# Optimization experiments

Measured on AMD Instinct MI355X. Metric: run time of the kernel, lower is better.

The kernel has to match this reference:

```python
import jax, jax.numpy as jnp
import numpy as np

NUM_ROUTING_ITERATIONS = 3


def _squash(t, axis=-1):
    # scale * t / ||t||, scale = ||t||^2 / (1 + ||t||^2)
    squared_norm = jnp.sum(t * t, axis=axis, keepdims=True)
    return squared_norm / (1.0 + squared_norm) * t / jnp.sqrt(squared_norm)


def setup_inputs() -> dict:
    key = jax.random.key(0)
    k_x, k_w = jax.random.split(key)
    B, R, C, O, I = 64, 2048, 16, 32, 16
    x = jax.random.normal(k_x, (B, R, I), dtype=jnp.float32)
    W = jax.random.normal(k_w, (R, C, O, I), dtype=jnp.float32)
    return {"x": x, "W": W}


def reference(x, W):
    # u_hat[b,r,c,o] = sum_i W[r,c,o,i] * x[b,r,i]
    u_hat = jnp.einsum('rcoi,bri->brco', W, x)  # [B,R,C,O]
    B, R, C, O = u_hat.shape
    b = jnp.zeros((B, R, C), dtype=u_hat.dtype)  # routing logits
    v = None
    for _ in range(NUM_ROUTING_ITERATIONS):
        c = jax.nn.softmax(b, axis=2)                      # softmax over capsules (dim=2)
        s = jnp.einsum('brc,brco->bro', c, u_hat)          # (c * u_hat).sum(dim=2)
        v = _squash(s, axis=-1)                            # [B,R,O]
        b = b + jnp.einsum('brco,bro->brc', u_hat, v)      # agreement update
    return v
```

## Files before the change

### kernel.cpp

```cpp
#include <hip/hip_runtime.h>

#define R_DIM 2048
#define O_DIM 32
#define I_DIM 16
#define B_DIM 64
#define BB 32

typedef _Float16 half8  __attribute__((ext_vector_type(8)));
typedef float    f32x4  __attribute__((ext_vector_type(4)));

struct SplitH { half8 h1, h2; };

__device__ __forceinline__ SplitH splitf16x8(const float* __restrict__ p) {
    float f[8];
    *(float4*)(f)     = *(const float4*)(p);
    *(float4*)(f + 4) = *(const float4*)(p + 4);
    SplitH r;
    #pragma unroll
    for (int j = 0; j < 4; ++j) {
        const auto a = __builtin_amdgcn_cvt_pkrtz(f[2*j], f[2*j+1]);
        const float r0 = f[2*j]     - (float)a[0];
        const float r1 = f[2*j + 1] - (float)a[1];
        const auto c = __builtin_amdgcn_cvt_pkrtz(r0, r1);
        r.h1[2*j] = (_Float16)a[0]; r.h1[2*j+1] = (_Float16)a[1];
        r.h2[2*j] = (_Float16)c[0]; r.h2[2*j+1] = (_Float16)c[1];
    }
    return r;
}

template<int CTRL>
__device__ __forceinline__ float dpp_mv(float v) {
    int t = __builtin_amdgcn_update_dpp(0, __float_as_int(v), CTRL, 0xf, 0xf, true);
    return __int_as_float(t);
}
__device__ __forceinline__ float row16_sum(float v) {
    v += dpp_mv<0xB1>(v);
    v += dpp_mv<0x4E>(v);
    v += dpp_mv<0x124>(v);
    v += dpp_mv<0x128>(v);
    return v;
}

__device__ __forceinline__ int swaddr(int b, int col) {
    return b * 512 + (col ^ (((b ^ (b >> 2)) & 3) << 3));
}

__global__ __launch_bounds__(512, 4)
void capsule_routing_kernel(const float* __restrict__ x,
                            const float* __restrict__ W,
                            float* __restrict__ out) {
    __shared__ float u_lds[BB * 512];

    const int tid = threadIdx.x;
    const int bid = blockIdx.x;
    const int r   = bid >> 1;
    const int b0  = (bid & 1) * BB;

    {
        const int lane = tid & 63;
        const int w    = tid >> 6;
        const int q    = lane >> 4;
        const int np   = lane & 15;

        const half8 z8 = {0,0,0,0,0,0,0,0};
        SplitH as[2];
        #pragma unroll
        for (int mt = 0; mt < 2; ++mt) {
            as[mt].h1 = z8; as[mt].h2 = z8;
            if (q < 2)
                as[mt] = splitf16x8(x + ((size_t)(b0 + mt * 16 + np) * R_DIM + r) * I_DIM + q * 8);
        }

        const f32x4 zero4 = {0.f, 0.f, 0.f, 0.f};
        #pragma unroll
        for (int t = 0; t < 4; ++t) {
            const int ntile = w * 4 + t;
            SplitH bs; bs.h1 = z8; bs.h2 = z8;
            if (q < 2)
                bs = splitf16x8(W + ((size_t)r * 512 + ntile * 16 + np) * I_DIM + q * 8);

            #pragma unroll
            for (int mt = 0; mt < 2; ++mt) {
                f32x4 a = __builtin_amdgcn_mfma_f32_16x16x32_f16(as[mt].h2, bs.h1, zero4, 0, 0, 0);
                a = __builtin_amdgcn_mfma_f32_16x16x32_f16(as[mt].h1, bs.h2, a, 0, 0, 0);
                a = __builtin_amdgcn_mfma_f32_16x16x32_f16(as[mt].h1, bs.h1, a, 0, 0, 0);
                const int col = ntile * 16 + np;
                #pragma unroll
                for (int reg = 0; reg < 4; ++reg)
                    u_lds[swaddr(mt * 16 + q * 4 + reg, col)] = a[reg];
            }
        }
    }
    __syncthreads();

    {
        const int b = tid >> 4;
        const int j = tid & 15;

        float u2[32];
        #pragma unroll
        for (int c = 0; c < 16; ++c) {
            const float2 v2 = *(const float2*)&u_lds[swaddr(b, c * 32 + 2 * j)];
            u2[2 * c]     = v2.x;
            u2[2 * c + 1] = v2.y;
        }

        float bv[16];
        #pragma unroll
        for (int c = 0; c < 16; ++c) bv[c] = 0.0f;

        float s0 = 0.f, s1 = 0.f, g = 0.f;

        #pragma unroll
        for (int it = 0; it < 3; ++it) {
            if (it == 0) {
                s0 = 0.f; s1 = 0.f;
                #pragma unroll
                for (int c = 0; c < 16; ++c) { s0 += u2[2*c]; s1 += u2[2*c+1]; }
                s0 *= 0.0625f; s1 *= 0.0625f;
            } else {
                float m = bv[0];
                #pragma unroll
                for (int c = 1; c < 16; ++c) m = fmaxf(m, bv[c]);
                float Z = 0.f; s0 = 0.f; s1 = 0.f;
                #pragma unroll
                for (int c = 0; c < 16; ++c) {
                    const float e = __expf(bv[c] - m);
                    Z += e;
                    s0 = fmaf(e, u2[2*c],   s0);
                    s1 = fmaf(e, u2[2*c+1], s1);
                }
                const float rZ = __builtin_amdgcn_rcpf(Z);
                s0 *= rZ; s1 *= rZ;
            }

            const float nn = row16_sum(s0 * s0 + s1 * s1);
            g = sqrtf(nn) * __builtin_amdgcn_rcpf(1.0f + nn);

            if (it < 2) {
                #pragma unroll
                for (int c = 0; c < 16; ++c) {
                    const float t = row16_sum(fmaf(u2[2*c], s0, u2[2*c+1] * s1));
                    bv[c] = fmaf(g, t, bv[c]);
                }
            }
        }

        *(float2*)(out + ((size_t)(b0 + b) * R_DIM + r) * O_DIM + 2 * j)
            = make_float2(g * s0, g * s1);
    }
}

extern "C" void kernel_launch(void* const* d_in, const int* in_sizes, int n_in,
                              void* d_out, int out_size, void* d_ws, size_t ws_size,
                              hipStream_t stream) {
    const float* x   = (const float*)d_in[0];
    const float* W   = (const float*)d_in[1];
    float*       out = (float*)d_out;

    dim3 grid(R_DIM * (B_DIM / BB));
    dim3 block(512);
    hipLaunchKernelGGL(capsule_routing_kernel, grid, block, 0, stream, x, W, out);
}
```

Baseline: 147.8 us.

## Distribute routing logits across lanes with DPP rotate-reduce and halve batch tile

Each of the 16 lanes in a row now owns one capsule's routing logit. The capsule index is skewed by lane so that the agreement reduction becomes a rotating DPP accumulate chain, replacing 16 separate row16_sum butterflies. The weighted sum is handled the same way by rotating the softmax weights. Softmax max and sum use row-wide DPP reductions instead of per-thread loops over 16 logits. The batch tile drops from 32 to 16 with 256-thread blocks, which doubles the grid and reloads W twice as often. The intent is to cut cross-lane reduction instructions and register pressure.

```diff
diff --git a/kernel.cpp b/kernel.cpp
--- a/kernel.cpp
+++ b/kernel.cpp
@@ -4,7 +4,7 @@
 #define O_DIM 32
 #define I_DIM 16
 #define B_DIM 64
-#define BB 32
+#define BB 16
 
 typedef _Float16 half8  __attribute__((ext_vector_type(8)));
 typedef float    f32x4  __attribute__((ext_vector_type(4)));
@@ -40,12 +40,20 @@
     v += dpp_mv<0x128>(v);
     return v;
 }
+__device__ __forceinline__ float row16_max(float v) {
+    v = fmaxf(v, dpp_mv<0xB1>(v));
+    v = fmaxf(v, dpp_mv<0x4E>(v));
+    v = fmaxf(v, dpp_mv<0x124>(v));
+    v = fmaxf(v, dpp_mv<0x128>(v));
+    return v;
+}
+__device__ __forceinline__ float ror1(float v) { return dpp_mv<0x121>(v); }
 
 __device__ __forceinline__ int swaddr(int b, int col) {
     return b * 512 + (col ^ (((b ^ (b >> 2)) & 3) << 3));
 }
 
-__global__ __launch_bounds__(512, 4)
+__global__ __launch_bounds__(256, 5)
 void capsule_routing_kernel(const float* __restrict__ x,
                             const float* __restrict__ W,
                             float* __restrict__ out) {
@@ -53,8 +61,8 @@
 
     const int tid = threadIdx.x;
     const int bid = blockIdx.x;
-    const int r   = bid >> 1;
-    const int b0  = (bid & 1) * BB;
+    const int r   = bid >> 2;
+    const int b0  = (bid & 3) * BB;
 
     {
         const int lane = tid & 63;
@@ -63,32 +71,26 @@
         const int np   = lane & 15;
 
         const half8 z8 = {0,0,0,0,0,0,0,0};
-        SplitH as[2];
-        #pragma unroll
-        for (int mt = 0; mt < 2; ++mt) {
-            as[mt].h1 = z8; as[mt].h2 = z8;
-            if (q < 2)
-                as[mt] = splitf16x8(x + ((size_t)(b0 + mt * 16 + np) * R_DIM + r) * I_DIM + q * 8);
-        }
+        SplitH as; as.h1 = z8; as.h2 = z8;
+        if (q < 2)
+            as = splitf16x8(x + ((size_t)(b0 + np) * R_DIM + r) * I_DIM + q * 8);
 
         const f32x4 zero4 = {0.f, 0.f, 0.f, 0.f};
         #pragma unroll
-        for (int t = 0; t < 4; ++t) {
-            const int ntile = w * 4 + t;
+        for (int t = 0; t < 8; ++t) {
+            const int ntile = w * 8 + t;
             SplitH bs; bs.h1 = z8; bs.h2 = z8;
             if (q < 2)
                 bs = splitf16x8(W + ((size_t)r * 512 + ntile * 16 + np) * I_DIM + q * 8);
 
+            f32x4 a = __builtin_amdgcn_mfma_f32_16x16x32_f16(as.h2, bs.h1, zero4, 0, 0, 0);
+            a = __builtin_amdgcn_mfma_f32_16x16x32_f16(as.h1, bs.h2, a, 0, 0, 0);
+            a = __builtin_amdgcn_mfma_f32_16x16x32_f16(as.h1, bs.h1, a, 0, 0, 0);
+
+            const int col = ntile * 16 + np;
             #pragma unroll
-            for (int mt = 0; mt < 2; ++mt) {
-                f32x4 a = __builtin_amdgcn_mfma_f32_16x16x32_f16(as[mt].h2, bs.h1, zero4, 0, 0, 0);
-                a = __builtin_amdgcn_mfma_f32_16x16x32_f16(as[mt].h1, bs.h2, a, 0, 0, 0);
-                a = __builtin_amdgcn_mfma_f32_16x16x32_f16(as[mt].h1, bs.h1, a, 0, 0, 0);
-                const int col = ntile * 16 + np;
-                #pragma unroll
-                for (int reg = 0; reg < 4; ++reg)
-                    u_lds[swaddr(mt * 16 + q * 4 + reg, col)] = a[reg];
-            }
+            for (int reg = 0; reg < 4; ++reg)
+                u_lds[swaddr(q * 4 + reg, col)] = a[reg];
         }
     }
     __syncthreads();
@@ -99,16 +101,14 @@
 
         float u2[32];
         #pragma unroll
-        for (int c = 0; c < 16; ++c) {
+        for (int k = 0; k < 16; ++k) {
+            const int c = (j - k) & 15;
             const float2 v2 = *(const float2*)&u_lds[swaddr(b, c * 32 + 2 * j)];
-            u2[2 * c]     = v2.x;
-            u2[2 * c + 1] = v2.y;
+            u2[2 * k]     = v2.x;
+            u2[2 * k + 1] = v2.y;
         }
 
-        float bv[16];
-        #pragma unroll
-        for (int c = 0; c < 16; ++c) bv[c] = 0.0f;
-
+        float bvv = 0.0f;
         float s0 = 0.f, s1 = 0.f, g = 0.f;
 
         #pragma unroll
@@ -116,33 +116,35 @@
             if (it == 0) {
                 s0 = 0.f; s1 = 0.f;
                 #pragma unroll
-                for (int c = 0; c < 16; ++c) { s0 += u2[2*c]; s1 += u2[2*c+1]; }
+                for (int k = 0; k < 16; ++k) { s0 += u2[2*k]; s1 += u2[2*k+1]; }
                 s0 *= 0.0625f; s1 *= 0.0625f;
             } else {
-                float m = bv[0];
+                const float m = row16_max(bvv);
+                const float e = __expf(bvv - m);
+                const float Z = row16_sum(e);
+                float wr = e * __builtin_amdgcn_rcpf(Z);
+                s0 = 0.f; s1 = 0.f;
                 #pragma unroll
-                for (int c = 1; c < 16; ++c) m = fmaxf(m, bv[c]);
-                float Z = 0.f; s0 = 0.f; s1 = 0.f;
-                #pragma unroll
-                for (int c = 0; c < 16; ++c) {
-                    const float e = __expf(bv[c] - m);
-                    Z += e;
-                    s0 = fmaf(e, u2[2*c],   s0);
-                    s1 = fmaf(e, u2[2*c+1], s1);
+                for (int k = 0; k < 16; ++k) {
+                    if (k > 0) wr = ror1(wr);
+                    s0 = fmaf(wr, u2[2*k],     s0);
+                    s1 = fmaf(wr, u2[2*k + 1], s1);
                 }
-                const float rZ = __builtin_amdgcn_rcpf(Z);
-                s0 *= rZ; s1 *= rZ;
             }
 
             const float nn = row16_sum(s0 * s0 + s1 * s1);
             g = sqrtf(nn) * __builtin_amdgcn_rcpf(1.0f + nn);
 
             if (it < 2) {
+                float acc = 0.f;
                 #pragma unroll
-                for (int c = 0; c < 16; ++c) {
-                    const float t = row16_sum(fmaf(u2[2*c], s0, u2[2*c+1] * s1));
-                    bv[c] = fmaf(g, t, bv[c]);
+                for (int k = 0; k < 16; ++k) {
+                    if (k > 0) acc = ror1(acc);
+                    acc = fmaf(u2[2*k],     s0, acc);
+                    acc = fmaf(u2[2*k + 1], s1, acc);
                 }
+                acc = ror1(acc);
+                bvv = fmaf(g, acc, bvv);
             }
         }
 
@@ -159,6 +161,6 @@
     float*       out = (float*)d_out;
 
     dim3 grid(R_DIM * (B_DIM / BB));
-    dim3 block(512);
+    dim3 block(256);
     hipLaunchKernelGGL(capsule_routing_kernel, grid, block, 0, stream, x, W, out);
 }
```

Result: slower. 150.8 us (+2.0%).
